# Optimization experiments

Hardware: AMD Instinct MI355X
Metric: run time of the kernel (lower is better)

## Reference

```python
import jax, jax.numpy as jnp
import numpy as np

B, N, D, DFF, E, K, H = 8, 1024, 512, 2048, 8, 2, 8


def setup_inputs() -> dict:
    key = jax.random.key(0)
    ks = jax.random.split(key, 20)
    p = lambda k, shape: (jax.random.normal(k, shape, jnp.float32) * 0.02)
    x = jax.random.normal(ks[0], (B, N, D), jnp.float32)
    adj = (jax.random.uniform(ks[1], (B, N, N)) > 0.5).astype(jnp.float32)
    return {
        "x": x,
        "adj": adj,
        "gc_w": p(ks[2], (D, D)),
        "gc_b": jnp.zeros((D,), jnp.float32),
        "root_emb": p(ks[3], (1, D)),
        "in_w": p(ks[4], (3 * D, D)),
        "in_b": jnp.zeros((3 * D,), jnp.float32),
        "out_w": p(ks[5], (D, D)),
        "out_b": jnp.zeros((D,), jnp.float32),
        "ln1_g": jnp.ones((D,), jnp.float32),
        "ln1_b": jnp.zeros((D,), jnp.float32),
        "ln2_g": jnp.ones((D,), jnp.float32),
        "ln2_b": jnp.zeros((D,), jnp.float32),
        "gate_w": p(ks[6], (E, D)),
        "W1": p(ks[7], (E, D, DFF)),
        "b1": jnp.zeros((E, DFF), jnp.float32),
        "W2": p(ks[8], (E, DFF, D)),
        "b2": jnp.zeros((E, D), jnp.float32),
    }


def layer_norm(x, g, b, eps=1e-5):
    mu = jnp.mean(x, axis=-1, keepdims=True)
    var = jnp.var(x, axis=-1, keepdims=True)
    return (x - mu) * jax.lax.rsqrt(var + eps) * g + b


def reference(x, adj, gc_w, gc_b, root_emb, in_w, in_b, out_w, out_b,
              ln1_g, ln1_b, ln2_g, ln2_b, gate_w, W1, b1, W2, b2):
    b, n, d = x.shape
    h = H
    hd = d // h
    # GraphConv: adj @ x -> linear -> + root embedding (index 0 for every batch)
    g = jnp.einsum('bij,bjd->bid', adj, x) @ gc_w.T + gc_b + root_emb[0]
    x = x + g
    # MultiheadAttention (self-attn, eval mode, no mask)
    qkv = x @ in_w.T + in_b                      # [B,N,3D]
    q, k, v = jnp.split(qkv, 3, axis=-1)
    to_heads = lambda t: t.reshape(b, n, h, hd).transpose(0, 2, 1, 3)
    q, k, v = to_heads(q), to_heads(k), to_heads(v)
    scale = jnp.float32(1.0) / jnp.sqrt(jnp.float32(hd))
    scores = jnp.einsum('bhqe,bhke->bhqk', q * scale, k)
    attn = jax.nn.softmax(scores, axis=-1)
    o = jnp.einsum('bhqk,bhke->bhqe', attn, v).transpose(0, 2, 1, 3).reshape(b, n, d)
    o = o @ out_w.T + out_b
    x = layer_norm(x + o, ln1_g, ln1_b)
    # MoE: top-k gating, normalized weights, weighted sum of expert FFN outputs
    xf = x.reshape(-1, d)                        # [T,D]
    t = xf.shape[0]
    gate_probs = jax.nn.softmax(xf @ gate_w.T, axis=-1)        # [T,E]
    topk_p, topk_i = jax.lax.top_k(gate_probs, K)
    topk_p = topk_p / jnp.sum(topk_p, axis=-1, keepdims=True)
    num_e = gate_w.shape[0]
    w = jnp.zeros((t, num_e), xf.dtype).at[jnp.arange(t)[:, None], topk_i].add(topk_p)
    hid = jax.nn.gelu(jnp.einsum('td,edf->etf', xf, W1) + b1[:, None, :], approximate=False)
    y = jnp.einsum('etf,efd->etd', hid, W2) + b2[:, None, :]   # [E,T,D]
    moe = jnp.einsum('te,etd->td', w, y).reshape(b, n, d)
    return layer_norm(x + moe, ln2_g, ln2_b)
```

## Files before the change

### kernel.cpp

```cpp
#include <hip/hip_runtime.h>
#include <hip/hip_bf16.h>

#define NB 8
#define NSEQ 1024
#define DMODEL 512
#define DF 2048
#define NEXP 8
#define NHEAD 8
#define HDIM 64
#define T_TOK (NB * NSEQ)

typedef unsigned short u16;
typedef float f32x4_t __attribute__((ext_vector_type(4)));
typedef __bf16 bf16x8_t __attribute__((ext_vector_type(8)));

__device__ __forceinline__ u16 f2b(float f) {
  __hip_bfloat16 h = __float2bfloat16(f);
  return *reinterpret_cast<u16*>(&h);
}
__device__ __forceinline__ float b2f(u16 u) {
  return __uint_as_float((unsigned)u << 16);
}
__device__ __forceinline__ void gl_lds16(const u16* g, u16* l) {
  __builtin_amdgcn_global_load_lds(
      (const __attribute__((address_space(1))) unsigned int*)g,
      (__attribute__((address_space(3))) unsigned int*)l, 16, 0, 0);
}

__global__ __launch_bounds__(256) void k_cvt_hl(const float* __restrict__ src,
                                                u16* __restrict__ hi,
                                                u16* __restrict__ lo, int n4) {
  const int i = blockIdx.x * 256 + threadIdx.x;
  if (i >= n4) return;
  const float4 v = ((const float4*)src)[i];
  ushort4 h, l;
  h.x = f2b(v.x); l.x = f2b(v.x - b2f(h.x));
  h.y = f2b(v.y); l.y = f2b(v.y - b2f(h.y));
  h.z = f2b(v.z); l.z = f2b(v.z - b2f(h.z));
  h.w = f2b(v.w); l.w = f2b(v.w - b2f(h.w));
  ((ushort4*)hi)[i] = h;
  ((ushort4*)lo)[i] = l;
}

__global__ __launch_bounds__(256) void k_cvt_b(const float* __restrict__ src,
                                               u16* __restrict__ dst, int n4) {
  const int i = blockIdx.x * 256 + threadIdx.x;
  if (i >= n4) return;
  const float4 v = ((const float4*)src)[i];
  ushort4 h;
  h.x = f2b(v.x); h.y = f2b(v.y); h.z = f2b(v.z); h.w = f2b(v.w);
  ((ushort4*)dst)[i] = h;
}

__global__ __launch_bounds__(256) void k_cvt_t_hl(const float* __restrict__ src,
                                                  u16* __restrict__ hi,
                                                  u16* __restrict__ lo,
                                                  int R, int C) {
  const int z = blockIdx.z;
  src += (size_t)z * R * C;
  hi += (size_t)z * R * C;
  lo += (size_t)z * R * C;
  const int r0 = blockIdx.y * 64, c0 = blockIdx.x * 64;
  __shared__ u16 th[64][65], tl[64][65];
  const int t = threadIdx.x;
  const int cc = t & 63, rb = t >> 6;
#pragma unroll
  for (int i = 0; i < 16; ++i) {
    const int r = i * 4 + rb;
    const float f = src[(size_t)(r0 + r) * C + c0 + cc];
    const u16 h = f2b(f);
    th[r][cc] = h;
    tl[r][cc] = f2b(f - b2f(h));
  }
  __syncthreads();
#pragma unroll
  for (int i = 0; i < 16; ++i) {
    const int r = i * 4 + rb;
    hi[(size_t)(c0 + r) * R + r0 + cc] = th[cc][r];
    lo[(size_t)(c0 + r) * R + r0 + cc] = tl[cc][r];
  }
}

template <int TERMS, int EP>
__global__ __launch_bounds__(256) void k_gemm_sp(
    const u16* __restrict__ Ah, const u16* __restrict__ Al,
    const u16* __restrict__ Bh, const u16* __restrict__ Bl,
    const float* __restrict__ bias, const float* __restrict__ addv,
    const float* __restrict__ addm, float* __restrict__ outF,
    u16* __restrict__ outH, u16* __restrict__ outL,
    u16* __restrict__ outVH, u16* __restrict__ outVL, int K, int N,
    size_t aStride, size_t bStride, size_t cStride) {
  const int z = blockIdx.z;
  Ah += (size_t)z * aStride;
  if (TERMS == 3) Al += (size_t)z * aStride;
  Bh += (size_t)z * bStride;
  Bl += (size_t)z * bStride;
  const int m0 = blockIdx.y * 128, n0 = blockIdx.x * 128;
  __shared__ u16 Ash[128][64];
  __shared__ u16 Asl[(TERMS == 3) ? 128 : 1][64];
  __shared__ u16 Bsh[128][64];
  __shared__ u16 Bsl[128][64];
  const int t = threadIdx.x;
  const int w = t >> 6, l = t & 63;
  const int srow = w * 8 + (l >> 3);
  const int sscol = ((l & 7) ^ (l >> 3)) * 8;
  size_t aoff[4], boff[4];
#pragma unroll
  for (int i = 0; i < 4; ++i) {
    aoff[i] = (size_t)(m0 + i * 32 + srow) * K + sscol;
    boff[i] = (size_t)(n0 + i * 32 + srow) * K + sscol;
  }
  const int wr = w >> 1, wc = w & 1;
  const int lr = l & 15, lg = l >> 4;
  f32x4_t acc[4][4] = {};
  for (int k0 = 0; k0 < K; k0 += 64) {
#pragma unroll
    for (int i = 0; i < 4; ++i) {
      gl_lds16(Ah + aoff[i] + k0, &Ash[i * 32 + w * 8][0]);
      if (TERMS == 3) gl_lds16(Al + aoff[i] + k0, &Asl[i * 32 + w * 8][0]);
      gl_lds16(Bh + boff[i] + k0, &Bsh[i * 32 + w * 8][0]);
      gl_lds16(Bl + boff[i] + k0, &Bsl[i * 32 + w * 8][0]);
    }
    __syncthreads();
#pragma unroll
    for (int kk = 0; kk < 2; ++kk) {
      const int cs = (kk * 32 + lg * 8) ^ ((lr & 7) << 3);
      bf16x8_t ah[4], al[4], bh[4], bl[4];
#pragma unroll
      for (int m = 0; m < 4; ++m) {
        ah[m] = *(const bf16x8_t*)&Ash[wr * 64 + m * 16 + lr][cs];
        if (TERMS == 3)
          al[m] = *(const bf16x8_t*)&Asl[wr * 64 + m * 16 + lr][cs];
      }
#pragma unroll
      for (int n = 0; n < 4; ++n) {
        bh[n] = *(const bf16x8_t*)&Bsh[wc * 64 + n * 16 + lr][cs];
        bl[n] = *(const bf16x8_t*)&Bsl[wc * 64 + n * 16 + lr][cs];
      }
#pragma unroll
      for (int m = 0; m < 4; ++m)
#pragma unroll
        for (int n = 0; n < 4; ++n) {
          acc[m][n] = __builtin_amdgcn_mfma_f32_16x16x32_bf16(ah[m], bh[n],
                                                              acc[m][n], 0, 0, 0);
          acc[m][n] = __builtin_amdgcn_mfma_f32_16x16x32_bf16(ah[m], bl[n],
                                                              acc[m][n], 0, 0, 0);
          if (TERMS == 3)
            acc[m][n] = __builtin_amdgcn_mfma_f32_16x16x32_bf16(
                al[m], bh[n], acc[m][n], 0, 0, 0);
        }
    }
    __syncthreads();
  }
  const size_t cb = (size_t)z * cStride;
#pragma unroll
  for (int m = 0; m < 4; ++m) {
#pragma unroll
    for (int n = 0; n < 4; ++n) {
      const int c = n0 + wc * 64 + n * 16 + lr;
#pragma unroll
      for (int j = 0; j < 4; ++j) {
        const int r = m0 + wr * 64 + m * 16 + lg * 4 + j;
        float v = acc[m][n][j];
        if (EP == 1) v += bias[c] + addv[c] + addm[(size_t)r * N + c];
        if (EP == 2 || EP == 4) v += bias[c];
        const size_t idx = cb + (size_t)r * N + c;
        if (EP == 1 || EP == 2) outF[idx] = v;
        if (EP == 0 || EP == 1) {
          const u16 h = f2b(v);
          outH[idx] = h;
          outL[idx] = f2b(v - b2f(h));
        }
        if (EP == 4) {
          if (c < DMODEL) v *= 0.125f;
          const u16 h = f2b(v);
          const u16 lo = f2b(v - b2f(h));
          if (c < 2 * DMODEL) {
            outH[idx] = h;
            outL[idx] = lo;
          } else {
            const int d = (c - 2 * DMODEL) & 63;
            const int hd = (c - 2 * DMODEL) >> 6;
            const int bb = r >> 10;
            const int tile = (r & 1023) >> 6;
            const int tv = r & 63;
            const int cc2 = 4 * (tv & 15) + (tv >> 4);
            const int stc = cc2 ^ ((d & 7) << 3);
            const size_t vo =
                (((size_t)(bb * 8 + hd) * 16 + tile) * 64 + d) * 64 + stc;
            outVH[vo] = h;
            outVL[vo] = lo;
          }
        }
      }
    }
  }
}

__global__ __launch_bounds__(256) void k_attn(const u16* __restrict__ qh_g,
                                              const u16* __restrict__ ql_g,
                                              const u16* __restrict__ vph,
                                              const u16* __restrict__ vpl,
                                              u16* __restrict__ oh_g,
                                              u16* __restrict__ ol_g) {
  const int q0 = blockIdx.x * 128, h = blockIdx.y, b = blockIdx.z;
  const int t = threadIdx.x;
  const int w = t >> 6, l = t & 63;
  const int lr = l & 15, lg = l >> 4;
  __shared__ u16 Ksh[64][64], Ksl[64][64];
  __shared__ u16 Vth[64][64], Vtl[64][64];
  __shared__ u16 Psh[128][64], Psl[128][64];
  u16* VthF = &Vth[0][0];
  u16* VtlF = &Vtl[0][0];
  bf16x8_t qh[2][2], ql[2][2];
#pragma unroll
  for (int s = 0; s < 2; ++s) {
    const size_t qoff =
        (size_t)(b * NSEQ + q0 + s * 64 + w * 16 + lr) * (3 * DMODEL) +
        h * HDIM;
#pragma unroll
    for (int kc = 0; kc < 2; ++kc) {
      qh[s][kc] = *(const bf16x8_t*)(qh_g + qoff + kc * 32 + lg * 8);
      ql[s][kc] = *(const bf16x8_t*)(ql_g + qoff + kc * 32 + lg * 8);
    }
  }
  float mrow[2][4], lrow[2][4];
#pragma unroll
  for (int s = 0; s < 2; ++s)
#pragma unroll
    for (int j = 0; j < 4; ++j) { mrow[s][j] = -1e30f; lrow[s][j] = 0.f; }
  f32x4_t acc_o[2][4] = {};
  const int sr = t >> 2;
  const int sc = (t & 3) * 16;
  const int cs0 = sc ^ ((sr & 7) << 3);
  const int cs1 = (sc + 8) ^ ((sr & 7) << 3);
  const size_t vbh = ((size_t)(b * 8 + h) * 16) * 4096;
  const int vsub = w * 512 + l * 8;
  uint4 pkh0, pkh1, pkl0, pkl1, pvh0, pvh1, pvl0, pvl1;
  {
    const size_t kro =
        (size_t)(b * NSEQ + sr) * (3 * DMODEL) + DMODEL + h * HDIM + sc;
    pkh0 = *(const uint4*)(qh_g + kro);
    pkh1 = *(const uint4*)(qh_g + kro + 8);
    pkl0 = *(const uint4*)(ql_g + kro);
    pkl1 = *(const uint4*)(ql_g + kro + 8);
    pvh0 = *(const uint4*)(vph + vbh + vsub);
    pvh1 = *(const uint4*)(vph + vbh + 2048 + vsub);
    pvl0 = *(const uint4*)(vpl + vbh + vsub);
    pvl1 = *(const uint4*)(vpl + vbh + 2048 + vsub);
  }
  for (int k0 = 0; k0 < NSEQ; k0 += 64) {
    __syncthreads();
    *(uint4*)&Ksh[sr][cs0] = pkh0;
    *(uint4*)&Ksh[sr][cs1] = pkh1;
    *(uint4*)&Ksl[sr][cs0] = pkl0;
    *(uint4*)&Ksl[sr][cs1] = pkl1;
    *(uint4*)(VthF + vsub) = pvh0;
    *(uint4*)(VthF + 2048 + vsub) = pvh1;
    *(uint4*)(VtlF + vsub) = pvl0;
    *(uint4*)(VtlF + 2048 + vsub) = pvl1;
    __syncthreads();
    if (k0 + 64 < NSEQ) {
      const size_t kro = (size_t)(b * NSEQ + k0 + 64 + sr) * (3 * DMODEL) +
                         DMODEL + h * HDIM + sc;
      pkh0 = *(const uint4*)(qh_g + kro);
      pkh1 = *(const uint4*)(qh_g + kro + 8);
      pkl0 = *(const uint4*)(ql_g + kro);
      pkl1 = *(const uint4*)(ql_g + kro + 8);
      const size_t vt = vbh + (size_t)((k0 >> 6) + 1) * 4096;
      pvh0 = *(const uint4*)(vph + vt + vsub);
      pvh1 = *(const uint4*)(vph + vt + 2048 + vsub);
      pvl0 = *(const uint4*)(vpl + vt + vsub);
      pvl1 = *(const uint4*)(vpl + vt + 2048 + vsub);
    }
    f32x4_t sacc[2][4] = {};
    __builtin_amdgcn_s_setprio(1);
#pragma unroll
    for (int kc = 0; kc < 2; ++kc) {
      const int cs = (kc * 32 + lg * 8) ^ ((lr & 7) << 3);
#pragma unroll
      for (int n = 0; n < 4; ++n) {
        const bf16x8_t kh = *(const bf16x8_t*)&Ksh[n * 16 + lr][cs];
        const bf16x8_t kl = *(const bf16x8_t*)&Ksl[n * 16 + lr][cs];
#pragma unroll
        for (int s = 0; s < 2; ++s) {
          sacc[s][n] = __builtin_amdgcn_mfma_f32_16x16x32_bf16(
              qh[s][kc], kh, sacc[s][n], 0, 0, 0);
          sacc[s][n] = __builtin_amdgcn_mfma_f32_16x16x32_bf16(
              qh[s][kc], kl, sacc[s][n], 0, 0, 0);
          sacc[s][n] = __builtin_amdgcn_mfma_f32_16x16x32_bf16(
              ql[s][kc], kh, sacc[s][n], 0, 0, 0);
        }
      }
    }
    __builtin_amdgcn_s_setprio(0);
#pragma unroll
    for (int s = 0; s < 2; ++s) {
      float alpha[4];
#pragma unroll
      for (int j = 0; j < 4; ++j) {
        float mx = fmaxf(fmaxf(sacc[s][0][j], sacc[s][1][j]),
                         fmaxf(sacc[s][2][j], sacc[s][3][j]));
        mx = fmaxf(mx, __shfl_xor(mx, 1));
        mx = fmaxf(mx, __shfl_xor(mx, 2));
        mx = fmaxf(mx, __shfl_xor(mx, 4));
        mx = fmaxf(mx, __shfl_xor(mx, 8));
        const float mnew = fmaxf(mrow[s][j], mx);
        alpha[j] = __expf(mrow[s][j] - mnew);
        mrow[s][j] = mnew;
        float psum = 0.f;
        const int prow = lg * 4 + j;
        ushort4 ph4, pl4;
        u16* php = (u16*)&ph4;
        u16* plp = (u16*)&pl4;
#pragma unroll
        for (int n = 0; n < 4; ++n) {
          const float p = __expf(sacc[s][n][j] - mnew);
          psum += p;
          const u16 hi = f2b(p);
          php[n] = hi;
          plp[n] = f2b(p - b2f(hi));
        }
        const int pc = (4 * lr) ^ ((prow & 7) << 3);
        *(ushort4*)&Psh[s * 64 + w * 16 + prow][pc] = ph4;
        *(ushort4*)&Psl[s * 64 + w * 16 + prow][pc] = pl4;
        psum += __shfl_xor(psum, 1);
        psum += __shfl_xor(psum, 2);
        psum += __shfl_xor(psum, 4);
        psum += __shfl_xor(psum, 8);
        lrow[s][j] = lrow[s][j] * alpha[j] + psum;
      }
#pragma unroll
      for (int n = 0; n < 4; ++n)
#pragma unroll
        for (int j = 0; j < 4; ++j) acc_o[s][n][j] *= alpha[j];
    }
    __builtin_amdgcn_s_setprio(1);
#pragma unroll
    for (int kc = 0; kc < 2; ++kc) {
      const int cs = (kc * 32 + lg * 8) ^ ((lr & 7) << 3);
      bf16x8_t ph[2], pl[2];
#pragma unroll
      for (int s = 0; s < 2; ++s) {
        ph[s] = *(const bf16x8_t*)&Psh[s * 64 + w * 16 + lr][cs];
        pl[s] = *(const bf16x8_t*)&Psl[s * 64 + w * 16 + lr][cs];
      }
#pragma unroll
      for (int n = 0; n < 4; ++n) {
        const bf16x8_t vh = *(const bf16x8_t*)&Vth[n * 16 + lr][cs];
        const bf16x8_t vl = *(const bf16x8_t*)&Vtl[n * 16 + lr][cs];
#pragma unroll
        for (int s = 0; s < 2; ++s) {
          acc_o[s][n] = __builtin_amdgcn_mfma_f32_16x16x32_bf16(
              ph[s], vh, acc_o[s][n], 0, 0, 0);
          acc_o[s][n] = __builtin_amdgcn_mfma_f32_16x16x32_bf16(
              ph[s], vl, acc_o[s][n], 0, 0, 0);
          acc_o[s][n] = __builtin_amdgcn_mfma_f32_16x16x32_bf16(
              pl[s], vh, acc_o[s][n], 0, 0, 0);
        }
      }
    }
    __builtin_amdgcn_s_setprio(0);
  }
#pragma unroll
  for (int s = 0; s < 2; ++s) {
#pragma unroll
    for (int j = 0; j < 4; ++j) {
      const float invl = 1.0f / lrow[s][j];
      const size_t ro =
          (size_t)(b * NSEQ + q0 + s * 64 + w * 16 + lg * 4 + j) * DMODEL +
          h * HDIM;
#pragma unroll
      for (int n = 0; n < 4; ++n) {
        const float v = acc_o[s][n][j] * invl;
        const u16 hh = f2b(v);
        oh_g[ro + n * 16 + lr] = hh;
        ol_g[ro + n * 16 + lr] = f2b(v - b2f(hh));
      }
    }
  }
}

__global__ __launch_bounds__(256) void k_ln_add(
    const float* __restrict__ a, const float* __restrict__ bsrc,
    const float* __restrict__ g, const float* __restrict__ be,
    float* __restrict__ outp, u16* __restrict__ outb) {
  const int tok = blockIdx.x;
  const int t = threadIdx.x;
  float2 v;
  {
    const float2 va = *(const float2*)(a + (size_t)tok * DMODEL + t * 2);
    const float2 vb = *(const float2*)(bsrc + (size_t)tok * DMODEL + t * 2);
    v.x = va.x + vb.x; v.y = va.y + vb.y;
  }
  float s1 = v.x + v.y, s2 = v.x * v.x + v.y * v.y;
#pragma unroll
  for (int o = 32; o; o >>= 1) { s1 += __shfl_down(s1, o); s2 += __shfl_down(s2, o); }
  __shared__ float sm1[4], sm2[4];
  if ((t & 63) == 0) { sm1[t >> 6] = s1; sm2[t >> 6] = s2; }
  __syncthreads();
  s1 = sm1[0] + sm1[1] + sm1[2] + sm1[3];
  s2 = sm2[0] + sm2[1] + sm2[2] + sm2[3];
  const float mean = s1 * (1.f / DMODEL);
  const float var = s2 * (1.f / DMODEL) - mean * mean;
  const float rstd = rsqrtf(var + 1e-5f);
  float2 o;
  o.x = (v.x - mean) * rstd * g[t * 2] + be[t * 2];
  o.y = (v.y - mean) * rstd * g[t * 2 + 1] + be[t * 2 + 1];
  *(float2*)(outp + (size_t)tok * DMODEL + t * 2) = o;
  ushort2 ob;
  ob.x = f2b(o.x); ob.y = f2b(o.y);
  *(ushort2*)(outb + (size_t)tok * DMODEL + t * 2) = ob;
}

__global__ __launch_bounds__(256) void k_gate(const float* __restrict__ x2,
                                              const float* __restrict__ gw,
                                              int* __restrict__ eidx,
                                              float* __restrict__ ewgt) {
  const int t = threadIdx.x;
  const int g = t >> 4;
  const int s = t & 15;
  const int tok = blockIdx.x * 16 + g;
  float acc[NEXP] = {};
  const float* px = x2 + (size_t)tok * DMODEL + s * 32;
  const float* pw = gw + s * 32;
#pragma unroll
  for (int i = 0; i < 32; i += 4) {
    const float4 xv = *(const float4*)(px + i);
#pragma unroll
    for (int e = 0; e < NEXP; ++e) {
      const float4 wv = *(const float4*)(pw + e * DMODEL + i);
      acc[e] += xv.x * wv.x + xv.y * wv.y + xv.z * wv.z + xv.w * wv.w;
    }
  }
#pragma unroll
  for (int e = 0; e < NEXP; ++e) {
    acc[e] += __shfl_xor(acc[e], 1);
    acc[e] += __shfl_xor(acc[e], 2);
    acc[e] += __shfl_xor(acc[e], 4);
    acc[e] += __shfl_xor(acc[e], 8);
  }
  if (s == 0) {
    int i0 = 0; float b0 = acc[0];
#pragma unroll
    for (int e = 1; e < NEXP; ++e) if (acc[e] > b0) { b0 = acc[e]; i0 = e; }
    int i1 = -1; float v1 = -1e30f;
#pragma unroll
    for (int e = 0; e < NEXP; ++e)
      if (e != i0 && acc[e] > v1) { v1 = acc[e]; i1 = e; }
    const float tt = __expf(v1 - b0);
    const float w0 = 1.f / (1.f + tt), w1 = tt / (1.f + tt);
    eidx[tok * 2] = i0; eidx[tok * 2 + 1] = i1;
    ewgt[tok * 2] = w0; ewgt[tok * 2 + 1] = w1;
  }
}

__global__ void k_zero(int* __restrict__ p, int n) {
  const int i = blockIdx.x * blockDim.x + threadIdx.x;
  if (i < n) p[i] = 0;
}

__global__ __launch_bounds__(256) void k_count(const int* __restrict__ eidx,
                                               int* __restrict__ ecnt) {
  __shared__ int cnt[NEXP];
  const int t = threadIdx.x;
  if (t < NEXP) cnt[t] = 0;
  __syncthreads();
  atomicAdd(&cnt[eidx[blockIdx.x * 256 + t]], 1);
  __syncthreads();
  if (t < NEXP) atomicAdd(&ecnt[t], cnt[t]);
}

__global__ void k_offsets(const int* __restrict__ ecnt,
                          int* __restrict__ eoff, int* __restrict__ blkmap) {
  if (threadIdx.x == 0) {
    int s = 0;
    for (int e = 0; e < NEXP; ++e) { eoff[e] = s; s += ecnt[e]; }
    int nb = 0;
    for (int e = 0; e < NEXP; ++e)
      for (int m0 = 0; m0 < ecnt[e]; m0 += 128)
        blkmap[1 + nb++] = e | (m0 << 4);
    blkmap[0] = nb;
  }
}

__global__ __launch_bounds__(256) void k_scatter(
    const int* __restrict__ eidx, const int* __restrict__ eoff,
    int* __restrict__ efill, int* __restrict__ rtok, int* __restrict__ t2s) {
  __shared__ int lcnt[NEXP];
  __shared__ int lbase[NEXP];
  const int t = threadIdx.x;
  if (t < NEXP) lcnt[t] = 0;
  __syncthreads();
  const int tok = blockIdx.x * 128 + (t >> 1);
  const int k = t & 1;
  const int e = eidx[tok * 2 + k];
  const int lpos = atomicAdd(&lcnt[e], 1);
  __syncthreads();
  if (t < NEXP) lbase[t] = atomicAdd(&efill[t], lcnt[t]);
  __syncthreads();
  const int slot = eoff[e] + lbase[e] + lpos;
  rtok[slot] = tok;
  t2s[tok * 2 + k] = slot;
}

__global__ __launch_bounds__(256) void k_cvt_t(const float* __restrict__ src,
                                               u16* __restrict__ dst,
                                               int R, int C) {
  const int e = blockIdx.z;
  src += (size_t)e * R * C;
  dst += (size_t)e * R * C;
  const int r0 = blockIdx.y * 64, c0 = blockIdx.x * 64;
  __shared__ u16 tile[64][65];
  const int t = threadIdx.x;
  const int cc = t & 63, rb = t >> 6;
#pragma unroll
  for (int i = 0; i < 16; ++i) {
    const int r = i * 4 + rb;
    tile[r][cc] = f2b(src[(size_t)(r0 + r) * C + c0 + cc]);
  }
  __syncthreads();
#pragma unroll
  for (int i = 0; i < 16; ++i) {
    const int r = i * 4 + rb;
    dst[(size_t)(c0 + r) * R + r0 + cc] = tile[cc][r];
  }
}

template <int MODE>
__global__ __launch_bounds__(256) void k_moe_mfma(
    const u16* __restrict__ Ab, const u16* __restrict__ Bb,
    const float* __restrict__ bias, const int* __restrict__ rtok,
    const int* __restrict__ ecnt, const int* __restrict__ eoff,
    const int* __restrict__ blkmap, u16* __restrict__ outp) {
  constexpr int K = (MODE == 0) ? DMODEL : DF;
  constexpr int N = (MODE == 0) ? DF : DMODEL;
  const int nb = blkmap[0];
  if ((int)blockIdx.y >= nb) return;
  const int ent = blkmap[1 + blockIdx.y];
  const int e = ent & 15;
  const int m0 = ent >> 4;
  const int cnt = ecnt[e];
  const int off = eoff[e];
  const int n0 = blockIdx.x * 128;
  const u16* Bw = Bb + (size_t)e * (size_t)K * N;
  __shared__ u16 As[128][64];
  __shared__ u16 Bs[128][64];
  const int t = threadIdx.x;
  const int w = t >> 6, l = t & 63;
  const int srow = w * 8 + (l >> 3);
  const int sscol = ((l & 7) ^ (l >> 3)) * 8;
  const u16* arow[4];
#pragma unroll
  for (int i = 0; i < 4; ++i) {
    const int r = m0 + i * 32 + srow;
    const int rr = (r < cnt) ? r : (cnt - 1);
    if (MODE == 0)
      arow[i] = Ab + (size_t)rtok[off + rr] * K + sscol;
    else
      arow[i] = Ab + ((size_t)off + rr) * K + sscol;
  }
  const u16* brow[4];
#pragma unroll
  for (int i = 0; i < 4; ++i)
    brow[i] = Bw + (size_t)(n0 + i * 32 + srow) * K + sscol;

  const int wr = w >> 1, wc = w & 1;
  const int lr = l & 15, lg = l >> 4;
  f32x4_t acc[4][4] = {};
  for (int k0 = 0; k0 < K; k0 += 64) {
#pragma unroll
    for (int i = 0; i < 4; ++i) {
      gl_lds16(arow[i] + k0, &As[i * 32 + w * 8][0]);
      gl_lds16(brow[i] + k0, &Bs[i * 32 + w * 8][0]);
    }
    __syncthreads();
#pragma unroll
    for (int kk = 0; kk < 2; ++kk) {
      const int cs = (kk * 32 + lg * 8) ^ ((lr & 7) << 3);
      bf16x8_t af[4], bfr[4];
#pragma unroll
      for (int m = 0; m < 4; ++m)
        af[m] = *(const bf16x8_t*)&As[wr * 64 + m * 16 + lr][cs];
#pragma unroll
      for (int n = 0; n < 4; ++n)
        bfr[n] = *(const bf16x8_t*)&Bs[wc * 64 + n * 16 + lr][cs];
#pragma unroll
      for (int m = 0; m < 4; ++m)
#pragma unroll
        for (int n = 0; n < 4; ++n)
          acc[m][n] = __builtin_amdgcn_mfma_f32_16x16x32_bf16(
              af[m], bfr[n], acc[m][n], 0, 0, 0);
    }
    __syncthreads();
  }
#pragma unroll
  for (int m = 0; m < 4; ++m) {
    const int rl0 = wr * 64 + m * 16 + lg * 4;
#pragma unroll
    for (int n = 0; n < 4; ++n) {
      const int gc = n0 + wc * 64 + n * 16 + lr;
      const float bv = bias[e * N + gc];
#pragma unroll
      for (int j = 0; j < 4; ++j) {
        const int r = m0 + rl0 + j;
        if (r < cnt) {
          float v = acc[m][n][j] + bv;
          if (MODE == 0) v = v * 0.5f * (1.f + erff(v * 0.70710678118f));
          outp[((size_t)off + r) * N + gc] = f2b(v);
        }
      }
    }
  }
}

__global__ __launch_bounds__(256) void k_ln2(
    const float* __restrict__ x2, const u16* __restrict__ ybuf,
    const int* __restrict__ t2s, const float* __restrict__ ewgt,
    const float* __restrict__ g, const float* __restrict__ be,
    float* __restrict__ outp) {
  const int tok = blockIdx.x;
  const int t = threadIdx.x;
  const int s0 = t2s[tok * 2], s1i = t2s[tok * 2 + 1];
  const float w0 = ewgt[tok * 2], w1 = ewgt[tok * 2 + 1];
  float2 v;
  {
    const float2 a = *(const float2*)(x2 + (size_t)tok * DMODEL + t * 2);
    const ushort2 y0 = *(const ushort2*)(ybuf + (size_t)s0 * DMODEL + t * 2);
    const ushort2 y1 = *(const ushort2*)(ybuf + (size_t)s1i * DMODEL + t * 2);
    v.x = a.x + w0 * b2f(y0.x) + w1 * b2f(y1.x);
    v.y = a.y + w0 * b2f(y0.y) + w1 * b2f(y1.y);
  }
  float sum1 = v.x + v.y, sum2 = v.x * v.x + v.y * v.y;
#pragma unroll
  for (int o = 32; o; o >>= 1) { sum1 += __shfl_down(sum1, o); sum2 += __shfl_down(sum2, o); }
  __shared__ float sm1[4], sm2[4];
  if ((t & 63) == 0) { sm1[t >> 6] = sum1; sm2[t >> 6] = sum2; }
  __syncthreads();
  sum1 = sm1[0] + sm1[1] + sm1[2] + sm1[3];
  sum2 = sm2[0] + sm2[1] + sm2[2] + sm2[3];
  const float mean = sum1 * (1.f / DMODEL);
  const float var = sum2 * (1.f / DMODEL) - mean * mean;
  const float rstd = rsqrtf(var + 1e-5f);
  float2 o;
  o.x = (v.x - mean) * rstd * g[t * 2] + be[t * 2];
  o.y = (v.y - mean) * rstd * g[t * 2 + 1] + be[t * 2 + 1];
  *(float2*)(outp + (size_t)tok * DMODEL + t * 2) = o;
}

extern "C" void kernel_launch(void* const* d_in, const int* in_sizes, int n_in,
                              void* d_out, int out_size, void* d_ws,
                              size_t ws_size, hipStream_t stream) {
  const float* x      = (const float*)d_in[0];
  const float* adj    = (const float*)d_in[1];
  const float* gc_w   = (const float*)d_in[2];
  const float* gc_b   = (const float*)d_in[3];
  const float* root   = (const float*)d_in[4];
  const float* in_w   = (const float*)d_in[5];
  const float* in_b   = (const float*)d_in[6];
  const float* out_w  = (const float*)d_in[7];
  const float* out_b  = (const float*)d_in[8];
  const float* ln1_g  = (const float*)d_in[9];
  const float* ln1_b  = (const float*)d_in[10];
  const float* ln2_g  = (const float*)d_in[11];
  const float* ln2_b  = (const float*)d_in[12];
  const float* gate_w = (const float*)d_in[13];
  const float* W1     = (const float*)d_in[14];
  const float* b1     = (const float*)d_in[15];
  const float* W2     = (const float*)d_in[16];
  const float* b2     = (const float*)d_in[17];
  float* outp = (float*)d_out;

  constexpr size_t MB = 1ull << 20;
  char* W = (char*)d_ws;
  u16*   adj_bf = (u16*)(W + 0);
  u16*   xht    = (u16*)(W + 16 * MB);
  u16*   xlt    = (u16*)(W + 24 * MB);
  u16*   axh    = (u16*)(W + 32 * MB);
  u16*   axl    = (u16*)(W + 40 * MB);
  float* x1     = (float*)(W + 48 * MB);
  u16*   x1h    = (u16*)(W + 64 * MB);
  u16*   x1l    = (u16*)(W + 72 * MB);
  u16*   qkvh   = (u16*)(W + 0);
  u16*   qkvl   = (u16*)(W + 24 * MB);
  u16*   vph    = (u16*)(W + 80 * MB);
  u16*   vpl    = (u16*)(W + 88 * MB);
  u16*   oatth  = (u16*)(W + 96 * MB);
  u16*   oattl  = (u16*)(W + 104 * MB);
  float* oproj  = (float*)(W + 0);
  float* x2     = (float*)(W + 96 * MB);
  u16*   Wxb    = (u16*)(W + 80 * MB);
  u16*   hid    = (u16*)(W + 16 * MB);
  u16*   ybuf   = (u16*)(W + 0);
  char*  misc   = W + 112 * MB;
  char*  Od     = (char*)d_out;
  u16*   gwh = (u16*)(Od + 0);
  u16*   gwl = (u16*)(Od + 512 * 1024);
  u16*   iwh = (u16*)(Od + 1 * MB);
  u16*   iwl = (u16*)(Od + 1 * MB + 1536 * 1024);
  u16*   owh = (u16*)(Od + 4 * MB);
  u16*   owl = (u16*)(Od + 4 * MB + 512 * 1024);
  u16*   x2b = (u16*)d_out;
  int*   eidx  = (int*)misc;
  float* ewgt  = (float*)(misc + 65536);
  int*   ecnt  = (int*)(misc + 131072);
  int*   eoff  = (int*)(misc + 131072 + 128);
  int*   efill = (int*)(misc + 131072 + 256);
  int*   rtok  = (int*)(misc + 131072 + 512);
  int*   t2s   = (int*)(misc + 131072 + 512 + 65536);
  int*   blkmap = (int*)(misc + 131072 + 512 + 131072);

  k_cvt_b<<<dim3(8192), 256, 0, stream>>>(adj, adj_bf, NB * NSEQ * NSEQ / 4);
  k_cvt_t_hl<<<dim3(8, 16, 8), 256, 0, stream>>>(x, xht, xlt, NSEQ, DMODEL);
  k_cvt_hl<<<dim3(256), 256, 0, stream>>>(gc_w, gwh, gwl, DMODEL * DMODEL / 4);
  k_cvt_hl<<<dim3(768), 256, 0, stream>>>(in_w, iwh, iwl, 3 * DMODEL * DMODEL / 4);
  k_cvt_hl<<<dim3(256), 256, 0, stream>>>(out_w, owh, owl, DMODEL * DMODEL / 4);
  k_gemm_sp<2, 0><<<dim3(4, 8, 8), 256, 0, stream>>>(
      adj_bf, nullptr, xht, xlt, nullptr, nullptr, nullptr, nullptr, axh, axl,
      nullptr, nullptr, NSEQ, DMODEL, (size_t)NSEQ * NSEQ,
      (size_t)DMODEL * NSEQ, (size_t)NSEQ * DMODEL);
  k_gemm_sp<3, 1><<<dim3(4, 64, 1), 256, 0, stream>>>(
      axh, axl, gwh, gwl, gc_b, root, x, x1, x1h, x1l, nullptr, nullptr,
      DMODEL, DMODEL, 0, 0, 0);
  k_gemm_sp<3, 4><<<dim3(12, 64, 1), 256, 0, stream>>>(
      x1h, x1l, iwh, iwl, in_b, nullptr, nullptr, nullptr, qkvh, qkvl, vph,
      vpl, DMODEL, 3 * DMODEL, 0, 0, 0);
  k_attn<<<dim3(8, 8, 8), 256, 0, stream>>>(qkvh, qkvl, vph, vpl, oatth,
                                            oattl);
  k_gemm_sp<3, 2><<<dim3(4, 64, 1), 256, 0, stream>>>(
      oatth, oattl, owh, owl, out_b, nullptr, nullptr, oproj, nullptr, nullptr,
      nullptr, nullptr, DMODEL, DMODEL, 0, 0, 0);
  k_ln_add<<<dim3(T_TOK), 256, 0, stream>>>(x1, oproj, ln1_g, ln1_b, x2, x2b);
  k_zero<<<dim3(1), 128, 0, stream>>>((int*)(misc + 131072), 128);
  k_gate<<<dim3(T_TOK / 16), 256, 0, stream>>>(x2, gate_w, eidx, ewgt);
  k_count<<<dim3(2 * T_TOK / 256), 256, 0, stream>>>(eidx, ecnt);
  k_offsets<<<dim3(1), 64, 0, stream>>>(ecnt, eoff, blkmap);
  k_scatter<<<dim3(T_TOK / 128), 256, 0, stream>>>(eidx, eoff, efill, rtok,
                                                   t2s);
  k_cvt_t<<<dim3(DF / 64, DMODEL / 64, NEXP), 256, 0, stream>>>(W1, Wxb,
                                                                DMODEL, DF);
  k_moe_mfma<0><<<dim3(DF / 128, 135, 1), 256, 0, stream>>>(
      x2b, Wxb, b1, rtok, ecnt, eoff, blkmap, hid);
  k_cvt_t<<<dim3(DMODEL / 64, DF / 64, NEXP), 256, 0, stream>>>(W2, Wxb, DF,
                                                                DMODEL);
  k_moe_mfma<1><<<dim3(DMODEL / 128, 135, 1), 256, 0, stream>>>(
      hid, Wxb, b2, rtok, ecnt, eoff, blkmap, ybuf);
  k_ln2<<<dim3(T_TOK), 256, 0, stream>>>(x2, ybuf, t2s, ewgt, ln2_g, ln2_b,
                                         outp);
}
```

Baseline: 502.6 us.

## Fuse MoE gating into LayerNorm kernel and widen MoE GEMM tile to 256 columns

```diff
diff --git a/kernel.cpp b/kernel.cpp
--- a/kernel.cpp
+++ b/kernel.cpp
@@ -384,7 +384,9 @@
 __global__ __launch_bounds__(256) void k_ln_add(
     const float* __restrict__ a, const float* __restrict__ bsrc,
     const float* __restrict__ g, const float* __restrict__ be,
-    float* __restrict__ outp, u16* __restrict__ outb) {
+    const float* __restrict__ gw, float* __restrict__ outp,
+    u16* __restrict__ outb, int* __restrict__ eidx,
+    float* __restrict__ ewgt) {
   const int tok = blockIdx.x;
   const int t = threadIdx.x;
   float2 v;
@@ -397,6 +399,7 @@
 #pragma unroll
   for (int o = 32; o; o >>= 1) { s1 += __shfl_down(s1, o); s2 += __shfl_down(s2, o); }
   __shared__ float sm1[4], sm2[4];
+  __shared__ float smg[4][NEXP];
   if ((t & 63) == 0) { sm1[t >> 6] = s1; sm2[t >> 6] = s2; }
   __syncthreads();
   s1 = sm1[0] + sm1[1] + sm1[2] + sm1[3];
@@ -411,43 +414,38 @@
   ushort2 ob;
   ob.x = f2b(o.x); ob.y = f2b(o.y);
   *(ushort2*)(outb + (size_t)tok * DMODEL + t * 2) = ob;
-}
-
-__global__ __launch_bounds__(256) void k_gate(const float* __restrict__ x2,
-                                              const float* __restrict__ gw,
-                                              int* __restrict__ eidx,
-                                              float* __restrict__ ewgt) {
-  const int t = threadIdx.x;
-  const int g = t >> 4;
-  const int s = t & 15;
-  const int tok = blockIdx.x * 16 + g;
-  float acc[NEXP] = {};
-  const float* px = x2 + (size_t)tok * DMODEL + s * 32;
-  const float* pw = gw + s * 32;
-#pragma unroll
-  for (int i = 0; i < 32; i += 4) {
-    const float4 xv = *(const float4*)(px + i);
-#pragma unroll
-    for (int e = 0; e < NEXP; ++e) {
-      const float4 wv = *(const float4*)(pw + e * DMODEL + i);
-      acc[e] += xv.x * wv.x + xv.y * wv.y + xv.z * wv.z + xv.w * wv.w;
-    }
-  }
+  float p[NEXP];
 #pragma unroll
   for (int e = 0; e < NEXP; ++e) {
-    acc[e] += __shfl_xor(acc[e], 1);
-    acc[e] += __shfl_xor(acc[e], 2);
-    acc[e] += __shfl_xor(acc[e], 4);
-    acc[e] += __shfl_xor(acc[e], 8);
-  }
-  if (s == 0) {
-    int i0 = 0; float b0 = acc[0];
-#pragma unroll
-    for (int e = 1; e < NEXP; ++e) if (acc[e] > b0) { b0 = acc[e]; i0 = e; }
+    const float2 wv = *(const float2*)(gw + e * DMODEL + t * 2);
+    p[e] = o.x * wv.x + o.y * wv.y;
+  }
+#pragma unroll
+  for (int e = 0; e < NEXP; ++e) {
+    p[e] += __shfl_xor(p[e], 1);
+    p[e] += __shfl_xor(p[e], 2);
+    p[e] += __shfl_xor(p[e], 4);
+    p[e] += __shfl_xor(p[e], 8);
+    p[e] += __shfl_xor(p[e], 16);
+    p[e] += __shfl_xor(p[e], 32);
+  }
+  if ((t & 63) == 0) {
+#pragma unroll
+    for (int e = 0; e < NEXP; ++e) smg[t >> 6][e] = p[e];
+  }
+  __syncthreads();
+  if (t == 0) {
+    float lg2[NEXP];
+#pragma unroll
+    for (int e = 0; e < NEXP; ++e)
+      lg2[e] = smg[0][e] + smg[1][e] + smg[2][e] + smg[3][e];
+    int i0 = 0; float b0 = lg2[0];
+#pragma unroll
+    for (int e = 1; e < NEXP; ++e) if (lg2[e] > b0) { b0 = lg2[e]; i0 = e; }
     int i1 = -1; float v1 = -1e30f;
 #pragma unroll
     for (int e = 0; e < NEXP; ++e)
-      if (e != i0 && acc[e] > v1) { v1 = acc[e]; i1 = e; }
+      if (e != i0 && lg2[e] > v1) { v1 = lg2[e]; i1 = e; }
     const float tt = __expf(v1 - b0);
     const float w0 = 1.f / (1.f + tt), w1 = tt / (1.f + tt);
     eidx[tok * 2] = i0; eidx[tok * 2 + 1] = i1;
@@ -542,10 +540,10 @@
   const int m0 = ent >> 4;
   const int cnt = ecnt[e];
   const int off = eoff[e];
-  const int n0 = blockIdx.x * 128;
+  const int n0 = blockIdx.x * 256;
   const u16* Bw = Bb + (size_t)e * (size_t)K * N;
   __shared__ u16 As[128][64];
-  __shared__ u16 Bs[128][64];
+  __shared__ u16 Bs[256][64];
   const int t = threadIdx.x;
   const int w = t >> 6, l = t & 63;
   const int srow = w * 8 + (l >> 3);
@@ -560,35 +558,36 @@
     else
       arow[i] = Ab + ((size_t)off + rr) * K + sscol;
   }
-  const u16* brow[4];
-#pragma unroll
-  for (int i = 0; i < 4; ++i)
+  const u16* brow[8];
+#pragma unroll
+  for (int i = 0; i < 8; ++i)
     brow[i] = Bw + (size_t)(n0 + i * 32 + srow) * K + sscol;
 
   const int wr = w >> 1, wc = w & 1;
   const int lr = l & 15, lg = l >> 4;
-  f32x4_t acc[4][4] = {};
+  f32x4_t acc[4][8] = {};
   for (int k0 = 0; k0 < K; k0 += 64) {
 #pragma unroll
-    for (int i = 0; i < 4; ++i) {
+    for (int i = 0; i < 4; ++i)
       gl_lds16(arow[i] + k0, &As[i * 32 + w * 8][0]);
+#pragma unroll
+    for (int i = 0; i < 8; ++i)
       gl_lds16(brow[i] + k0, &Bs[i * 32 + w * 8][0]);
-    }
     __syncthreads();
 #pragma unroll
     for (int kk = 0; kk < 2; ++kk) {
       const int cs = (kk * 32 + lg * 8) ^ ((lr & 7) << 3);
-      bf16x8_t af[4], bfr[4];
+      bf16x8_t af[4], bfr[8];
 #pragma unroll
       for (int m = 0; m < 4; ++m)
         af[m] = *(const bf16x8_t*)&As[wr * 64 + m * 16 + lr][cs];
 #pragma unroll
-      for (int n = 0; n < 4; ++n)
-        bfr[n] = *(const bf16x8_t*)&Bs[wc * 64 + n * 16 + lr][cs];
+      for (int n = 0; n < 8; ++n)
+        bfr[n] = *(const bf16x8_t*)&Bs[wc * 128 + n * 16 + lr][cs];
 #pragma unroll
       for (int m = 0; m < 4; ++m)
 #pragma unroll
-        for (int n = 0; n < 4; ++n)
+        for (int n = 0; n < 8; ++n)
           acc[m][n] = __builtin_amdgcn_mfma_f32_16x16x32_bf16(
               af[m], bfr[n], acc[m][n], 0, 0, 0);
     }
@@ -598,8 +597,8 @@
   for (int m = 0; m < 4; ++m) {
     const int rl0 = wr * 64 + m * 16 + lg * 4;
 #pragma unroll
-    for (int n = 0; n < 4; ++n) {
-      const int gc = n0 + wc * 64 + n * 16 + lr;
+    for (int n = 0; n < 8; ++n) {
+      const int gc = n0 + wc * 128 + n * 16 + lr;
       const float bv = bias[e * N + gc];
 #pragma unroll
       for (int j = 0; j < 4; ++j) {
@@ -730,20 +729,20 @@
   k_gemm_sp<3, 2><<<dim3(4, 64, 1), 256, 0, stream>>>(
       oatth, oattl, owh, owl, out_b, nullptr, nullptr, oproj, nullptr, nullptr,
       nullptr, nullptr, DMODEL, DMODEL, 0, 0, 0);
-  k_ln_add<<<dim3(T_TOK), 256, 0, stream>>>(x1, oproj, ln1_g, ln1_b, x2, x2b);
+  k_ln_add<<<dim3(T_TOK), 256, 0, stream>>>(x1, oproj, ln1_g, ln1_b, gate_w,
+                                            x2, x2b, eidx, ewgt);
   k_zero<<<dim3(1), 128, 0, stream>>>((int*)(misc + 131072), 128);
-  k_gate<<<dim3(T_TOK / 16), 256, 0, stream>>>(x2, gate_w, eidx, ewgt);
   k_count<<<dim3(2 * T_TOK / 256), 256, 0, stream>>>(eidx, ecnt);
   k_offsets<<<dim3(1), 64, 0, stream>>>(ecnt, eoff, blkmap);
   k_scatter<<<dim3(T_TOK / 128), 256, 0, stream>>>(eidx, eoff, efill, rtok,
                                                    t2s);
   k_cvt_t<<<dim3(DF / 64, DMODEL / 64, NEXP), 256, 0, stream>>>(W1, Wxb,
                                                                 DMODEL, DF);
-  k_moe_mfma<0><<<dim3(DF / 128, 135, 1), 256, 0, stream>>>(
+  k_moe_mfma<0><<<dim3(DF / 256, 135, 1), 256, 0, stream>>>(
       x2b, Wxb, b1, rtok, ecnt, eoff, blkmap, hid);
   k_cvt_t<<<dim3(DMODEL / 64, DF / 64, NEXP), 256, 0, stream>>>(W2, Wxb, DF,
                                                                 DMODEL);
-  k_moe_mfma<1><<<dim3(DMODEL / 128, 135, 1), 256, 0, stream>>>(
+  k_moe_mfma<1><<<dim3(DMODEL / 256, 135, 1), 256, 0, stream>>>(
       hid, Wxb, b2, rtok, ecnt, eoff, blkmap, ybuf);
   k_ln2<<<dim3(T_TOK), 256, 0, stream>>>(x2, ybuf, t2s, ewgt, ln2_g, ln2_b,
                                          outp);
```

New measurement: 609.9 us. 21.4% more time.
